# Performance work log

Measured on AMD Instinct MI355X. Metric: run time of the kernel, lower is better.

The kernel has to match this reference:

```python
import jax, jax.numpy as jnp
import numpy as np

WINDOW = (8, 8)
NUM_HEADS = 6
PAD_H, PAD_W = WINDOW[0] // 2, WINDOW[1] // 2


def window_partition(x, wh, ww):
    # x: (B, C, H, W) -> (B*nh*nw, wh*ww, C)
    B, C, H, W = x.shape
    nh, nw = H // wh, W // ww
    x = x.reshape(B, C, nh, wh, nw, ww)
    x = x.transpose(0, 2, 4, 3, 5, 1)  # B, nh, nw, wh, ww, C
    return x.reshape(B * nh * nw, wh * ww, C)


def window_merge(x, B, C, H, W, wh, ww):
    # x: (B*nh*nw, wh*ww, C) -> (B, C, H, W)
    nh, nw = H // wh, W // ww
    x = x.reshape(B, nh, nw, wh, ww, C)
    x = x.transpose(0, 5, 1, 3, 2, 4)  # B, C, nh, wh, nw, ww
    return x.reshape(B, C, H, W)


def window_mha(t, num_heads):
    # t: (Bn, N, 3*C) packed qkv -> (Bn, N, C)
    Bn, N, C3 = t.shape
    C = C3 // 3
    d = C // num_heads
    q, k, v = jnp.split(t, 3, axis=-1)
    to_heads = lambda u: u.reshape(Bn, N, num_heads, d).transpose(0, 2, 1, 3)
    q, k, v = to_heads(q), to_heads(k), to_heads(v)
    scale = 1.0 / np.sqrt(d)
    attn = jax.nn.softmax(jnp.einsum('bhnd,bhmd->bhnm', q, k) * scale, axis=-1)
    o = jnp.einsum('bhnm,bhmd->bhnd', attn, v)
    return o.transpose(0, 2, 1, 3).reshape(Bn, N, C)


def setup_inputs() -> dict:
    key = jax.random.key(0)
    ks = jax.random.split(key, 5)
    B, C, H, W = 4, 384, 128, 128
    Cq = 64 * NUM_HEADS  # qkv_dim * num_heads = 384
    return {
        'x': jax.random.normal(ks[0], (B, C, H, W), dtype=jnp.float32),
        'w_qkv': jax.random.normal(ks[1], (3 * Cq, C), dtype=jnp.float32) * 0.02,
        'b_qkv': jax.random.normal(ks[2], (3 * Cq,), dtype=jnp.float32) * 0.02,
        'w_head': jax.random.normal(ks[3], (C, Cq), dtype=jnp.float32) * 0.02,
        'b_head': jax.random.normal(ks[4], (C,), dtype=jnp.float32) * 0.02,
    }


def reference(x, w_qkv, b_qkv, w_head, b_head):
    B, C, H, W = x.shape
    wh, ww = WINDOW
    # 1x1 conv qkv projection
    qkv = jnp.einsum('bchw,oc->bohw', x, w_qkv) + b_qkv[None, :, None, None]
    Cq = qkv.shape[1] // 3
    # branch 1: unpadded windows
    x1 = window_partition(qkv, wh, ww)
    x1 = window_mha(x1, NUM_HEADS)
    x1 = window_merge(x1, B, Cq, H, W, wh, ww)
    # branch 2: pad by half window, windows, then crop back
    qkv_p = jnp.pad(qkv, ((0, 0), (0, 0), (PAD_H, PAD_H), (PAD_W, PAD_W)))
    Hp, Wp = H + 2 * PAD_H, W + 2 * PAD_W
    x2 = window_partition(qkv_p, wh, ww)
    x2 = window_mha(x2, NUM_HEADS)
    x2 = window_merge(x2, B, Cq, Hp, Wp, wh, ww)
    x2 = x2[:, :, PAD_H:Hp - PAD_H, PAD_W:Wp - PAD_W]
    # merge + 1x1 conv head projection
    out = jnp.einsum('bchw,oc->bohw', x1 + x2, w_head) + b_head[None, :, None, None]
    return out
```

## Files before the change

kernel.cpp:

```cpp
#include <hip/hip_runtime.h>

typedef __bf16 bf16x8 __attribute__((ext_vector_type(8)));
typedef float f32x4 __attribute__((ext_vector_type(4)));

#define HW 16384
#define QKV_C 1152
#define SP 66

union U4B8 { uint4 u; bf16x8 v; __bf16 h[8]; };
union U2B4 { uint2 u; __bf16 h[4]; };

__global__ __launch_bounds__(256) void k_qkv(const float* __restrict__ x,
    const float* __restrict__ wq, const float* __restrict__ bq,
    __bf16* __restrict__ qkv)
{
    __shared__ __bf16 As[128 * 72];
    __shared__ __bf16 Bs[128 * 72];
    const int tid = threadIdx.x;
    const int hw0 = blockIdx.x * 128;
    const int o0  = blockIdx.y * 128;
    const int b   = blockIdx.z;
    const float* xb = x + (size_t)b * 384 * HW;

    f32x4 acc[4][4];
#pragma unroll
    for (int i = 0; i < 4; ++i)
#pragma unroll
        for (int j = 0; j < 4; ++j)
#pragma unroll
            for (int e = 0; e < 4; ++e) acc[i][j][e] = 0.0f;

    const int l = tid & 63;
    const int wv = tid >> 6;
    const int wm = wv & 1;
    const int wn = wv >> 1;
    const int l16 = l & 15, quad = l >> 4;

    for (int kt = 0; kt < 6; ++kt) {
        const int c0 = kt * 64;
#pragma unroll
        for (int it = 0; it < 8; ++it) {
            int unit = it * 256 + tid;
            int o = unit >> 4, ch = unit & 15;
            float4 f = *(const float4*)(wq + (size_t)(o0 + o) * 384 + c0 + ch * 4);
            U2B4 t;
            t.h[0] = (__bf16)f.x; t.h[1] = (__bf16)f.y;
            t.h[2] = (__bf16)f.z; t.h[3] = (__bf16)f.w;
            *(uint2*)(As + o * 72 + ch * 4) = t.u;
        }
#pragma unroll
        for (int ph = 0; ph < 4; ++ph) {
            int unit = ph * 256 + tid;
            int hw = unit & 127, c8 = unit >> 7;
            const float* xp = xb + (size_t)(c0 + c8 * 8) * HW + hw0 + hw;
            U4B8 t;
#pragma unroll
            for (int j = 0; j < 8; ++j) t.h[j] = (__bf16)xp[(size_t)j * HW];
            *(uint4*)(Bs + hw * 72 + c8 * 8) = t.u;
        }
        __syncthreads();
#pragma unroll
        for (int ks = 0; ks < 2; ++ks) {
            bf16x8 a[4], bb[4];
#pragma unroll
            for (int t = 0; t < 4; ++t)
                a[t] = *(const bf16x8*)(As + (wm * 64 + t * 16 + l16) * 72 + ks * 32 + quad * 8);
#pragma unroll
            for (int t = 0; t < 4; ++t)
                bb[t] = *(const bf16x8*)(Bs + (wn * 64 + t * 16 + l16) * 72 + ks * 32 + quad * 8);
#pragma unroll
            for (int mt = 0; mt < 4; ++mt)
#pragma unroll
                for (int nt = 0; nt < 4; ++nt)
                    acc[mt][nt] = __builtin_amdgcn_mfma_f32_16x16x32_bf16(
                        a[mt], bb[nt], acc[mt][nt], 0, 0, 0);
        }
        __syncthreads();
    }

    __bf16* qb = qkv + (size_t)b * HW * QKV_C;
#pragma unroll
    for (int mt = 0; mt < 4; ++mt) {
        int oo = o0 + wm * 64 + mt * 16 + quad * 4;
        float4 bias = *(const float4*)(bq + oo);
#pragma unroll
        for (int nt = 0; nt < 4; ++nt) {
            int hw = hw0 + wn * 64 + nt * 16 + l16;
            U2B4 t;
            t.h[0] = (__bf16)(acc[mt][nt][0] + bias.x);
            t.h[1] = (__bf16)(acc[mt][nt][1] + bias.y);
            t.h[2] = (__bf16)(acc[mt][nt][2] + bias.z);
            t.h[3] = (__bf16)(acc[mt][nt][3] + bias.w);
            *(uint2*)(qb + (size_t)hw * QKV_C + oo) = t.u;
        }
    }
}

__global__ __launch_bounds__(192) void k_attn(const __bf16* __restrict__ qkv,
    __bf16* __restrict__ y1, __bf16* __restrict__ y2)
{
    __shared__ __bf16 sm[3][2][64 * SP];
    const int tid = threadIdx.x;
    const int l = tid & 63, wv = tid >> 6;
    const int wid = blockIdx.x * 3 + wv;
    const bool shifted = wid >= 6144;
    const int w2 = shifted ? wid - 6144 : wid;
    const int head = w2 % 6;
    const int win = w2 / 6;
    const int nw = shifted ? 17 : 16;
    const int wx = win % nw;
    const int t2 = win / nw;
    const int wy = t2 % nw;
    const int b  = t2 / nw;
    const int h0 = wy * 8 - (shifted ? 4 : 0);
    const int w0 = wx * 8 - (shifted ? 4 : 0);
    const __bf16* qb = qkv + (size_t)b * HW * QKV_C;
    __bf16* VT = &sm[wv][0][0];
    __bf16* P  = &sm[wv][1][0];
    const int l16 = l & 15, quad = l >> 4;
    const int cbase = head * 64;

#pragma unroll
    for (int it = 0; it < 8; ++it) {
        int unit = it * 64 + l;
        int tok = unit >> 3, c8 = unit & 7;
        int hh = h0 + (tok >> 3), ww = w0 + (tok & 7);
        U4B8 t;
        if ((unsigned)hh < 128u && (unsigned)ww < 128u)
            t.u = *(const uint4*)(qb + (size_t)(hh * 128 + ww) * QKV_C + 768 + cbase + c8 * 8);
        else
            t.u = make_uint4(0, 0, 0, 0);
#pragma unroll
        for (int e = 0; e < 8; ++e) VT[(c8 * 8 + e) * SP + tok] = t.h[e];
    }

    size_t toff[4]; bool tval[4];
#pragma unroll
    for (int t = 0; t < 4; ++t) {
        int tok = t * 16 + l16;
        int hh = h0 + (tok >> 3), ww = w0 + (tok & 7);
        tval[t] = ((unsigned)hh < 128u && (unsigned)ww < 128u);
        toff[t] = tval[t] ? (size_t)(hh * 128 + ww) * QKV_C : 0;
    }

    f32x4 s[4][4];
#pragma unroll
    for (int i = 0; i < 4; ++i)
#pragma unroll
        for (int j = 0; j < 4; ++j)
#pragma unroll
            for (int e = 0; e < 4; ++e) s[i][j][e] = 0.0f;

#pragma unroll
    for (int ks = 0; ks < 2; ++ks) {
        bf16x8 aq[4], bk[4];
#pragma unroll
        for (int t = 0; t < 4; ++t) {
            U4B8 uq, uk;
            if (tval[t]) {
                uq.u = *(const uint4*)(qb + toff[t] + cbase + ks * 32 + quad * 8);
                uk.u = *(const uint4*)(qb + toff[t] + 384 + cbase + ks * 32 + quad * 8);
            } else {
                uq.u = make_uint4(0, 0, 0, 0);
                uk.u = make_uint4(0, 0, 0, 0);
            }
            aq[t] = uq.v;
            bk[t] = uk.v;
        }
#pragma unroll
        for (int mt = 0; mt < 4; ++mt)
#pragma unroll
            for (int nt = 0; nt < 4; ++nt)
                s[mt][nt] = __builtin_amdgcn_mfma_f32_16x16x32_bf16(
                    aq[mt], bk[nt], s[mt][nt], 0, 0, 0);
    }

#pragma unroll
    for (int mt = 0; mt < 4; ++mt) {
#pragma unroll
        for (int e = 0; e < 4; ++e) {
            float m_ = fmaxf(fmaxf(s[mt][0][e], s[mt][1][e]),
                             fmaxf(s[mt][2][e], s[mt][3][e]));
#pragma unroll
            for (int st = 1; st < 16; st <<= 1) m_ = fmaxf(m_, __shfl_xor(m_, st, 64));
            float p[4];
#pragma unroll
            for (int nt = 0; nt < 4; ++nt) p[nt] = __expf((s[mt][nt][e] - m_) * 0.125f);
            float sum = p[0] + p[1] + p[2] + p[3];
#pragma unroll
            for (int st = 1; st < 16; st <<= 1) sum += __shfl_xor(sum, st, 64);
            float r = __fdividef(1.0f, sum);
            int row = mt * 16 + quad * 4 + e;
#pragma unroll
            for (int nt = 0; nt < 4; ++nt)
                P[row * SP + nt * 16 + l16] = (__bf16)(p[nt] * r);
        }
    }
    __syncthreads();

    f32x4 o[4][4];
#pragma unroll
    for (int i = 0; i < 4; ++i)
#pragma unroll
        for (int j = 0; j < 4; ++j)
#pragma unroll
            for (int e = 0; e < 4; ++e) o[i][j][e] = 0.0f;

#pragma unroll
    for (int ks = 0; ks < 2; ++ks) {
        bf16x8 ap[4], bvv[4];
#pragma unroll
        for (int t = 0; t < 4; ++t)
            ap[t] = *(const bf16x8*)(P + (t * 16 + l16) * SP + ks * 32 + quad * 8);
#pragma unroll
        for (int t = 0; t < 4; ++t)
            bvv[t] = *(const bf16x8*)(VT + (t * 16 + l16) * SP + ks * 32 + quad * 8);
#pragma unroll
        for (int mt = 0; mt < 4; ++mt)
#pragma unroll
            for (int nt = 0; nt < 4; ++nt)
                o[mt][nt] = __builtin_amdgcn_mfma_f32_16x16x32_bf16(
                    ap[mt], bvv[nt], o[mt][nt], 0, 0, 0);
    }
    __syncthreads();

#pragma unroll
    for (int mt = 0; mt < 4; ++mt)
#pragma unroll
        for (int e = 0; e < 4; ++e) {
            int row = mt * 16 + quad * 4 + e;
#pragma unroll
            for (int nt = 0; nt < 4; ++nt)
                VT[row * SP + nt * 16 + l16] = (__bf16)o[mt][nt][e];
        }
    __syncthreads();

    __bf16* yb = (shifted ? y2 : y1) + (size_t)b * HW * 384;
#pragma unroll
    for (int it = 0; it < 8; ++it) {
        int unit = it * 64 + l;
        int tok = unit >> 3, c8 = unit & 7;
        int hh = h0 + (tok >> 3), ww = w0 + (tok & 7);
        if ((unsigned)hh < 128u && (unsigned)ww < 128u)
            *(uint4*)(yb + (size_t)(hh * 128 + ww) * 384 + cbase + c8 * 8) =
                *(const uint4*)(VT + tok * SP + c8 * 8);
    }
}

__global__ __launch_bounds__(256) void k_head(const __bf16* __restrict__ y1,
    const __bf16* __restrict__ y2, const float* __restrict__ wh,
    const float* __restrict__ bh, float* __restrict__ out)
{
    __shared__ __bf16 As[128 * 72];
    __shared__ __bf16 Bs[128 * 72];
    const int tid = threadIdx.x;
    const int hw0 = blockIdx.x * 128;
    const int o0  = blockIdx.y * 128;
    const int b   = blockIdx.z;
    const __bf16* y1b = y1 + (size_t)b * HW * 384;
    const __bf16* y2b = y2 + (size_t)b * HW * 384;

    f32x4 acc[4][4];
#pragma unroll
    for (int i = 0; i < 4; ++i)
#pragma unroll
        for (int j = 0; j < 4; ++j)
#pragma unroll
            for (int e = 0; e < 4; ++e) acc[i][j][e] = 0.0f;

    const int l = tid & 63, wv = tid >> 6;
    const int wm = wv & 1;
    const int wn = wv >> 1;
    const int l16 = l & 15, quad = l >> 4;

    for (int kt = 0; kt < 6; ++kt) {
        const int c0 = kt * 64;
#pragma unroll
        for (int it = 0; it < 4; ++it) {
            int unit = it * 256 + tid;
            int hw = unit >> 3, c8 = unit & 7;
            size_t off = (size_t)(hw0 + hw) * 384 + c0 + c8 * 8;
            U4B8 t1, t2, r;
            t1.u = *(const uint4*)(y1b + off);
            t2.u = *(const uint4*)(y2b + off);
#pragma unroll
            for (int e = 0; e < 8; ++e)
                r.h[e] = (__bf16)((float)t1.h[e] + (float)t2.h[e]);
            *(uint4*)(As + hw * 72 + c8 * 8) = r.u;
        }
#pragma unroll
        for (int it = 0; it < 8; ++it) {
            int unit = it * 256 + tid;
            int o = unit >> 4, ch = unit & 15;
            float4 f = *(const float4*)(wh + (size_t)(o0 + o) * 384 + c0 + ch * 4);
            U2B4 t;
            t.h[0] = (__bf16)f.x; t.h[1] = (__bf16)f.y;
            t.h[2] = (__bf16)f.z; t.h[3] = (__bf16)f.w;
            *(uint2*)(Bs + o * 72 + ch * 4) = t.u;
        }
        __syncthreads();
#pragma unroll
        for (int ks = 0; ks < 2; ++ks) {
            bf16x8 a[4], bb[4];
#pragma unroll
            for (int t = 0; t < 4; ++t)
                a[t] = *(const bf16x8*)(As + (wm * 64 + t * 16 + l16) * 72 + ks * 32 + quad * 8);
#pragma unroll
            for (int t = 0; t < 4; ++t)
                bb[t] = *(const bf16x8*)(Bs + (wn * 64 + t * 16 + l16) * 72 + ks * 32 + quad * 8);
#pragma unroll
            for (int mt = 0; mt < 4; ++mt)
#pragma unroll
                for (int nt = 0; nt < 4; ++nt)
                    acc[mt][nt] = __builtin_amdgcn_mfma_f32_16x16x32_bf16(
                        a[mt], bb[nt], acc[mt][nt], 0, 0, 0);
        }
        __syncthreads();
    }

#pragma unroll
    for (int nt = 0; nt < 4; ++nt) {
        int oo = o0 + wn * 64 + nt * 16 + l16;
        float bb_ = bh[oo];
        float* ob = out + ((size_t)b * 384 + oo) * HW + hw0 + wm * 64;
#pragma unroll
        for (int mt = 0; mt < 4; ++mt) {
            float4 f;
            f.x = acc[mt][nt][0] + bb_;
            f.y = acc[mt][nt][1] + bb_;
            f.z = acc[mt][nt][2] + bb_;
            f.w = acc[mt][nt][3] + bb_;
            *(float4*)(ob + mt * 16 + quad * 4) = f;
        }
    }
}

extern "C" void kernel_launch(void* const* d_in, const int* in_sizes, int n_in,
                              void* d_out, int out_size, void* d_ws, size_t ws_size,
                              hipStream_t stream) {
    const float* x  = (const float*)d_in[0];
    const float* wq = (const float*)d_in[1];
    const float* bq = (const float*)d_in[2];
    const float* wh = (const float*)d_in[3];
    const float* bh = (const float*)d_in[4];
    float* out = (float*)d_out;

    __bf16* qkv = (__bf16*)d_ws;
    __bf16* y1  = qkv + (size_t)4 * HW * QKV_C;
    __bf16* y2  = y1 + (size_t)4 * HW * 384;

    k_qkv<<<dim3(128, 9, 4), 256, 0, stream>>>(x, wq, bq, qkv);
    k_attn<<<dim3(4360), 192, 0, stream>>>(qkv, y1, y2);
    k_head<<<dim3(128, 3, 4), 256, 0, stream>>>(y1, y2, wh, bh, out);
}
```

Before: 495.5 us.

## Pre-transpose x to bf16 and stream GEMM tiles via direct global-to-LDS loads

```diff
diff --git a/kernel.cpp b/kernel.cpp
--- a/kernel.cpp
+++ b/kernel.cpp
@@ -10,17 +10,68 @@
 union U4B8 { uint4 u; bf16x8 v; __bf16 h[8]; };
 union U2B4 { uint2 u; __bf16 h[4]; };
 
-__global__ __launch_bounds__(256) void k_qkv(const float* __restrict__ x,
-    const float* __restrict__ wq, const float* __restrict__ bq,
+__device__ __forceinline__ void gload_lds16(const __bf16* g, __bf16* l) {
+    __builtin_amdgcn_global_load_lds(
+        (const __attribute__((address_space(1))) unsigned int*)g,
+        (__attribute__((address_space(3))) unsigned int*)l, 16, 0, 0);
+}
+
+__global__ __launch_bounds__(256) void k_xt(const float* __restrict__ x,
+    __bf16* __restrict__ xT)
+{
+    __shared__ __bf16 T[64 * 68];
+    const int tid = threadIdx.x;
+    const int hw0 = blockIdx.x * 64;
+    const int c0  = blockIdx.y * 64;
+    const int b   = blockIdx.z;
+    const float* xb = x + (size_t)b * 384 * HW;
+#pragma unroll
+    for (int it = 0; it < 4; ++it) {
+        int unit = it * 256 + tid;
+        int c = unit >> 4, q = unit & 15;
+        float4 f = *(const float4*)(xb + (size_t)(c0 + c) * HW + hw0 + q * 4);
+        U2B4 t;
+        t.h[0] = (__bf16)f.x; t.h[1] = (__bf16)f.y;
+        t.h[2] = (__bf16)f.z; t.h[3] = (__bf16)f.w;
+        *(uint2*)(T + c * 68 + q * 4) = t.u;
+    }
+    __syncthreads();
+    __bf16* xtb = xT + (size_t)b * HW * 384;
+#pragma unroll
+    for (int it = 0; it < 2; ++it) {
+        int unit = it * 256 + tid;
+        int hw = unit >> 3, c8 = unit & 7;
+        U4B8 t;
+#pragma unroll
+        for (int j = 0; j < 8; ++j) t.h[j] = T[(c8 * 8 + j) * 68 + hw];
+        *(uint4*)(xtb + (size_t)(hw0 + hw) * 384 + c0 + c8 * 8) = t.u;
+    }
+}
+
+__global__ __launch_bounds__(256) void k_wconv(const float* __restrict__ wq,
+    __bf16* __restrict__ wqb)
+{
+    int idx = (blockIdx.x * 256 + threadIdx.x) * 8;
+    float4 f0 = *(const float4*)(wq + idx);
+    float4 f1 = *(const float4*)(wq + idx + 4);
+    U4B8 t;
+    t.h[0] = (__bf16)f0.x; t.h[1] = (__bf16)f0.y;
+    t.h[2] = (__bf16)f0.z; t.h[3] = (__bf16)f0.w;
+    t.h[4] = (__bf16)f1.x; t.h[5] = (__bf16)f1.y;
+    t.h[6] = (__bf16)f1.z; t.h[7] = (__bf16)f1.w;
+    *(uint4*)(wqb + idx) = t.u;
+}
+
+__global__ __launch_bounds__(256) void k_qkv(const __bf16* __restrict__ xT,
+    const __bf16* __restrict__ wqb, const float* __restrict__ bq,
     __bf16* __restrict__ qkv)
 {
-    __shared__ __bf16 As[128 * 72];
-    __shared__ __bf16 Bs[128 * 72];
+    __shared__ __bf16 As[128 * 64];
+    __shared__ __bf16 Bs[128 * 64];
     const int tid = threadIdx.x;
     const int hw0 = blockIdx.x * 128;
     const int o0  = blockIdx.y * 128;
     const int b   = blockIdx.z;
-    const float* xb = x + (size_t)b * 384 * HW;
 
     f32x4 acc[4][4];
 #pragma unroll
@@ -36,27 +87,18 @@
     const int wn = wv >> 1;
     const int l16 = l & 15, quad = l >> 4;
 
+    const __bf16* wrow = wqb + (size_t)o0 * 384;
+    const __bf16* xrow = xT + (size_t)b * HW * 384 + (size_t)hw0 * 384;
+    const int r = tid >> 3, c8 = (tid & 7) * 8;
+
     for (int kt = 0; kt < 6; ++kt) {
         const int c0 = kt * 64;
 #pragma unroll
-        for (int it = 0; it < 8; ++it) {
+        for (int it = 0; it < 4; ++it) {
             int unit = it * 256 + tid;
-            int o = unit >> 4, ch = unit & 15;
-            float4 f = *(const float4*)(wq + (size_t)(o0 + o) * 384 + c0 + ch * 4);
-            U2B4 t;
-            t.h[0] = (__bf16)f.x; t.h[1] = (__bf16)f.y;
-            t.h[2] = (__bf16)f.z; t.h[3] = (__bf16)f.w;
-            *(uint2*)(As + o * 72 + ch * 4) = t.u;
-        }
-#pragma unroll
-        for (int ph = 0; ph < 4; ++ph) {
-            int unit = ph * 256 + tid;
-            int hw = unit & 127, c8 = unit >> 7;
-            const float* xp = xb + (size_t)(c0 + c8 * 8) * HW + hw0 + hw;
-            U4B8 t;
-#pragma unroll
-            for (int j = 0; j < 8; ++j) t.h[j] = (__bf16)xp[(size_t)j * HW];
-            *(uint4*)(Bs + hw * 72 + c8 * 8) = t.u;
+            int rr = r + it * 32;
+            gload_lds16(wrow + (size_t)rr * 384 + c0 + c8, As + unit * 8);
+            gload_lds16(xrow + (size_t)rr * 384 + c0 + c8, Bs + unit * 8);
         }
         __syncthreads();
 #pragma unroll
@@ -64,10 +106,10 @@
             bf16x8 a[4], bb[4];
 #pragma unroll
             for (int t = 0; t < 4; ++t)
-                a[t] = *(const bf16x8*)(As + (wm * 64 + t * 16 + l16) * 72 + ks * 32 + quad * 8);
+                a[t] = *(const bf16x8*)(As + (wm * 64 + t * 16 + l16) * 64 + ks * 32 + quad * 8);
 #pragma unroll
             for (int t = 0; t < 4; ++t)
-                bb[t] = *(const bf16x8*)(Bs + (wn * 64 + t * 16 + l16) * 72 + ks * 32 + quad * 8);
+                bb[t] = *(const bf16x8*)(Bs + (wn * 64 + t * 16 + l16) * 64 + ks * 32 + quad * 8);
 #pragma unroll
             for (int mt = 0; mt < 4; ++mt)
 #pragma unroll
@@ -348,8 +390,12 @@
     __bf16* qkv = (__bf16*)d_ws;
     __bf16* y1  = qkv + (size_t)4 * HW * QKV_C;
     __bf16* y2  = y1 + (size_t)4 * HW * 384;
-
-    k_qkv<<<dim3(128, 9, 4), 256, 0, stream>>>(x, wq, bq, qkv);
-    k_attn<<<dim3(4360), 192, 0, stream>>>(qkv, y1, y2);
-    k_head<<<dim3(128, 3, 4), 256, 0, stream>>>(y1, y2, wh, bh, out);
-}
+    __bf16* xT  = y1;
+    __bf16* wqb = y2;
+
+    k_xt   <<<dim3(256, 6, 4), 256, 0, stream>>>(x, xT);
+    k_wconv<<<dim3(216),       256, 0, stream>>>(wq, wqb);
+    k_qkv  <<<dim3(128, 9, 4), 256, 0, stream>>>(xT, wqb, bq, qkv);
+    k_attn <<<dim3(4360),      192, 0, stream>>>(qkv, y1, y2);
+    k_head <<<dim3(128, 3, 4), 256, 0, stream>>>(y1, y2, wh, bh, out);
+}
```

After: 481.9 us. -2.7%, faster.
